# Kernel optimization log

Hardware: AMD Instinct MI355X
Metric: run time of the kernel (lower is better)

The kernel has to match this reference:

```python
import jax, jax.numpy as jnp
import numpy as np

B, N, E = 2, 16384, 262144          # batch, nodes, directed edges (avg deg 16)
K, D, Wm = 256, 3, 1                # nmodes, ndims, nmeasures
C, L, FC = 128, 4, 128              # channels, Fourier layers, fc hidden
IN_DIM, OUT_DIM = 3, 1


def setup_inputs() -> dict:
    key = jax.random.key(0)
    ks = jax.random.split(key, 20)
    s = 1.0 / (C * C)
    inp = {
        "x": jax.random.normal(ks[0], (B, N, IN_DIM), jnp.float32),
        "nodes": jax.random.uniform(ks[1], (B, N, D), jnp.float32),
        "node_mask": jnp.ones((B, N, 1), jnp.float32),
        "node_weights": jax.random.uniform(ks[2], (B, N, Wm), jnp.float32) / N,
        "directed_edges": jax.random.randint(ks[3], (B, E, 2), 0, N),
        "edge_gradient_weights": jax.random.normal(ks[4], (B, E, D), jnp.float32),
        "modes": jax.random.normal(ks[5], (K, D, Wm), jnp.float32),
        "sp_L": jnp.ones((D, Wm), jnp.float32),
        "weights_c": s * jax.random.uniform(ks[6], (L, C, C, K, Wm), jnp.float32),
        "weights_s": s * jax.random.uniform(ks[7], (L, C, C, K, Wm), jnp.float32),
        "weights_0": s * jax.random.uniform(ks[8], (L, C, C, 1, Wm), jnp.float32),
        "fc0_w": jax.random.normal(ks[9], (C, IN_DIM), jnp.float32) * 0.1,
        "fc0_b": jnp.zeros((C,), jnp.float32),
        "ws_w": jax.random.normal(ks[10], (L, C, C), jnp.float32) * 0.05,
        "ws_b": jnp.zeros((L, C), jnp.float32),
        "gws_w": jax.random.normal(ks[11], (L, C, D * C), jnp.float32) * 0.05,
        "gws_b": jnp.zeros((L, C), jnp.float32),
        "fc1_w": jax.random.normal(ks[12], (FC, C), jnp.float32) * 0.05,
        "fc1_b": jnp.zeros((FC,), jnp.float32),
        "fc2_w": jax.random.normal(ks[13], (OUT_DIM, FC), jnp.float32) * 0.05,
        "fc2_b": jnp.zeros((OUT_DIM,), jnp.float32),
    }
    return inp


def _gelu(x):
    return jax.nn.gelu(x, approximate=False)  # torch F.gelu default = exact erf


def _compute_gradient(f, directed_edges, edge_gradient_weights):
    # f: [B, C, N] -> gradients [B, C*D, N] via directed-edge scatter-add
    fT = jnp.transpose(f, (0, 2, 1))                       # [B, N, C]
    tgt, src = directed_edges[..., 0], directed_edges[..., 1]
    f_src = jnp.take_along_axis(fT, src[..., None], axis=1)  # [B, E, C]
    f_tgt = jnp.take_along_axis(fT, tgt[..., None], axis=1)
    msg = jnp.einsum('bed,bec->becd', edge_gradient_weights, f_src - f_tgt)
    msg = msg.reshape(msg.shape[0], msg.shape[1], -1)        # [B, E, C*D]

    def scat(m, t):
        return jnp.zeros((fT.shape[1], m.shape[-1]), m.dtype).at[t].add(m)

    g = jax.vmap(scat)(msg, tgt)                             # [B, N, C*D]
    return jnp.transpose(g, (0, 2, 1))


def _spectral_conv(x, wc, wsn, w0, bc, bs, b0, wbc, wbs, wb0):
    # x: [B, C_in, N]
    xc = jnp.einsum('bix,bxkw->bikw', x, wbc)
    xs = -jnp.einsum('bix,bxkw->bikw', x, wbs)
    x0 = jnp.einsum('bix,bxkw->bikw', x, wb0)
    fc = jnp.einsum('bikw,iokw->bokw', xc, wc) - jnp.einsum('bikw,iokw->bokw', xs, wsn)
    fs = jnp.einsum('bikw,iokw->bokw', xs, wc) + jnp.einsum('bikw,iokw->bokw', xc, wsn)
    f0 = jnp.einsum('bikw,iokw->bokw', x0, w0)
    return (jnp.einsum('bokw,bxkw->box', f0, b0)
            + 2.0 * jnp.einsum('bokw,bxkw->box', fc, bc)
            - 2.0 * jnp.einsum('bokw,bxkw->box', fs, bs))


def reference(x, nodes, node_mask, node_weights, directed_edges, edge_gradient_weights,
              modes, sp_L, weights_c, weights_s, weights_0,
              fc0_w, fc0_b, ws_w, ws_b, gws_w, gws_b, fc1_w, fc1_b, fc2_w, fc2_b):
    # Fourier bases with learnable length-scale sp_L: [K,D,Wm]*[D,Wm]
    temp = jnp.einsum('bxd,kdw->bxkw', nodes, modes * sp_L)   # [B,N,K,Wm]
    bc, bs = jnp.cos(temp), jnp.sin(temp)
    b0 = jnp.zeros((temp.shape[0], temp.shape[1], 1, temp.shape[3]), temp.dtype)
    nw = (node_weights * node_mask)[:, :, None, :]            # [B,N,1,Wm]
    wbc, wbs, wb0 = bc * nw, bs * nw, b0 * nw

    h = jnp.einsum('bxi,ci->bxc', x, fc0_w) + fc0_b           # lift [B,N,C]
    h = jnp.transpose(h, (0, 2, 1))                           # [B,C,N]

    for i in range(L):
        x1 = _spectral_conv(h, weights_c[i], weights_s[i], weights_0[i],
                            bc, bs, b0, wbc, wbs, wb0)
        x2 = jnp.einsum('oc,bcn->bon', ws_w[i], h) + ws_b[i][None, :, None]
        grad = _compute_gradient(h, directed_edges, edge_gradient_weights)
        x3 = jnp.einsum('og,bgn->bon', gws_w[i], grad) + gws_b[i][None, :, None]
        h = x1 + x2 + x3
        if i != L - 1:
            h = _gelu(h)

    h = jnp.transpose(h, (0, 2, 1))                           # [B,N,C]
    h = _gelu(jnp.einsum('bnc,fc->bnf', h, fc1_w) + fc1_b)
    out = jnp.einsum('bnf,of->bno', h, fc2_w) + fc2_b         # [B,N,out_dim]
    return out
```

## Files before the change

kernel.cpp:

```cpp
#include <hip/hip_runtime.h>
#include <math.h>

#define Bn 2
#define Nn 16384
#define En 262144
#define Kn 256
#define Cn 128
#define Rn 512
#define Ln 4
#define LDP 72
#define NSPLIT 32

typedef float f32x4 __attribute__((ext_vector_type(4)));
typedef short s16x8 __attribute__((ext_vector_type(8)));

__device__ __forceinline__ float gelu_f(float x){
  return 0.5f*x*(1.0f + erff(x*0.70710678118654752440f));
}
__device__ __forceinline__ unsigned short f2b(float x){
  unsigned int u = __float_as_uint(x);
  unsigned int r = (u + 0x7FFFu + ((u>>16)&1u)) >> 16;
  return (unsigned short)r;
}
__device__ __forceinline__ float b2f(unsigned short h){
  return __uint_as_float(((unsigned int)h)<<16);
}
__device__ __forceinline__ unsigned int pack2(float lo, float hi){
  return (unsigned int)f2b(lo) | ((unsigned int)f2b(hi) << 16);
}


__global__ __launch_bounds__(256) void k_nw(const float* __restrict__ nwt,
                                            const float* __restrict__ msk,
                                            float* __restrict__ nw){
  int i = blockIdx.x*256 + threadIdx.x;
  nw[i] = nwt[i]*msk[i];
}

__global__ __launch_bounds__(256) void k_basis(const float* __restrict__ nodes,
                                               const float* __restrict__ modes,
                                               const float* __restrict__ spl,
                                               unsigned short* __restrict__ basis,
                                               unsigned short* __restrict__ basisT){
  __shared__ unsigned short tile[32*520];
  int gn0 = blockIdx.x*32;
  int tid = threadIdx.x;
  float m0 = modes[tid*3+0]*spl[0];
  float m1 = modes[tid*3+1]*spl[1];
  float m2 = modes[tid*3+2]*spl[2];
  for (int j=0;j<32;j++){
    const float* nd = nodes + (size_t)(gn0+j)*3;
    float t = nd[0]*m0 + nd[1]*m1 + nd[2]*m2;
    float s,c;
    sincosf(t,&s,&c);
    tile[j*520 + tid]       = f2b(c);
    tile[j*520 + 256 + tid] = f2b(s);
  }
  __syncthreads();
  int row = tid>>3, col0 = (tid&7)*64;
  #pragma unroll
  for (int q=0;q<8;q++){
    s16x8 v = *(const s16x8*)&tile[row*520 + col0 + q*8];
    *(s16x8*)(basis + (size_t)(gn0+row)*Rn + col0 + q*8) = v;
  }
  int b = gn0 >> 14;
  int nl = gn0 & (Nn-1);
  #pragma unroll
  for (int h=0; h<2; h++){
    int r = h*256 + tid;
    unsigned short* dst = basisT + ((size_t)(b*Rn + r))*Nn + nl;
    #pragma unroll
    for (int q=0;q<4;q++){
      unsigned short tmp[8];
      #pragma unroll
      for (int e=0;e<8;e++) tmp[e] = tile[(q*8+e)*520 + r];
      *(s16x8*)(dst + q*8) = *(const s16x8*)tmp;
    }
  }
}

__global__ __launch_bounds__(256) void k_lift(const float* __restrict__ x,
                                              const float* __restrict__ w,
                                              const float* __restrict__ bias,
                                              const float* __restrict__ nw,
                                              unsigned short* __restrict__ hg,
                                              unsigned short* __restrict__ hpack,
                                              unsigned short* __restrict__ hwT){
  __shared__ float ht[64*132];
  int gn0 = blockIdx.x*64;
  int tid = threadIdx.x;
  int c = tid & 127, rh = tid >> 7;
  float w0 = w[c*3], w1 = w[c*3+1], w2 = w[c*3+2], bb = bias[c];
  for (int j=0;j<32;j++){
    int n = rh*32 + j;
    const float* xp = x + (size_t)(gn0+n)*3;
    float v = bb + xp[0]*w0 + xp[1]*w1 + xp[2]*w2;
    ht[n*132 + c] = v;
    unsigned short hv = f2b(v);
    hg[(size_t)(gn0+n)*Rn + c] = hv;
    hpack[(size_t)(gn0+n)*Cn + c] = hv;
  }
  __syncthreads();
  int b = gn0 >> 14, nl = gn0 & (Nn-1);
  int cc = tid>>1, hf = tid&1;
  unsigned short* dst = hwT + ((size_t)(b*Cn + cc))*Nn + nl + hf*32;
  #pragma unroll
  for (int q=0;q<8;q++){
    int n = hf*32 + q*4;
    float4 nv = *(const float4*)&nw[(size_t)b*Nn + nl + n];
    ushort4 pk;
    pk.x = f2b(ht[(n+0)*132+cc]*nv.x);
    pk.y = f2b(ht[(n+1)*132+cc]*nv.y);
    pk.z = f2b(ht[(n+2)*132+cc]*nv.z);
    pk.w = f2b(ht[(n+3)*132+cc]*nv.w);
    *(ushort4*)(dst + q*4) = pk;
  }
}

__global__ __launch_bounds__(128) void k_w2c(const float* __restrict__ ws_w,
                                             const float* __restrict__ ws_b,
                                             const float* __restrict__ gws_w,
                                             const float* __restrict__ gws_b,
                                             unsigned short* __restrict__ W2,
                                             float* __restrict__ bias2){
  int bid = blockIdx.x;
  int tid = threadIdx.x;
  unsigned short* wrow = W2 + (size_t)bid*Rn;
  wrow[tid] = f2b(ws_w[(size_t)bid*Cn + tid]);
  const float* g = gws_w + (size_t)bid*384;
  wrow[128+tid] = f2b(g[tid*3+0]);
  wrow[256+tid] = f2b(g[tid*3+1]);
  wrow[384+tid] = f2b(g[tid*3+2]);
  if (tid==0) bias2[bid] = ws_b[bid] + gws_b[bid];
}

__global__ __launch_bounds__(256) void k_cvt(const float* __restrict__ in,
                                             unsigned short* __restrict__ out, int n){
  int i = blockIdx.x*256 + threadIdx.x;
  if (i < n) out[i] = f2b(in[i]);
}


__global__ __launch_bounds__(256) void k_count(const int* __restrict__ de,
                                               int* __restrict__ cnt){
  int i = blockIdx.x*256 + threadIdx.x;
  int b = i >> 18;
  int tgt = de[(size_t)i*2];
  atomicAdd(&cnt[b*Nn + tgt], 1);
}

__global__ __launch_bounds__(1024) void k_scan(const int* __restrict__ cnt,
                                               int* __restrict__ rowptr,
                                               int* __restrict__ cursor){
  __shared__ int part[1024];
  int t = threadIdx.x;
  int b = t >> 9;
  int li = t & 511;
  int loc[32];
  int s = 0;
  int base = b*Nn + li*32;
  #pragma unroll
  for (int j=0;j<32;j++){ loc[j] = s; s += cnt[base+j]; }
  part[t] = s;
  __syncthreads();
  int run = s;
  for (int off=1; off<512; off<<=1){
    int v = (li >= off) ? part[t-off] : 0;
    __syncthreads();
    part[t] += v;
    __syncthreads();
  }
  int incl = part[t];
  int excl = incl - run;
  int rbase = b*(Nn+1) + li*32;
  #pragma unroll
  for (int j=0;j<32;j++){
    int val = excl + loc[j];
    rowptr[rbase+j] = val;
    cursor[base+j]  = val;
  }
  if (li == 511) rowptr[b*(Nn+1) + Nn] = incl;
}

__global__ __launch_bounds__(256) void k_fill(const int* __restrict__ de,
                                              const float* __restrict__ egw,
                                              int* __restrict__ cursor,
                                              float4* __restrict__ epack){
  int i = blockIdx.x*256 + threadIdx.x;
  int b = i >> 18;
  int tgt = de[(size_t)i*2];
  int src = de[(size_t)i*2+1];
  int pos = atomicAdd(&cursor[b*Nn + tgt], 1);
  const float* g = egw + (size_t)i*3;
  float4 pk;
  pk.x = __int_as_float(src);
  pk.y = g[0]; pk.z = g[1]; pk.w = g[2];
  epack[(size_t)b*En + pos] = pk;
}

__global__ __launch_bounds__(128) void k_grad(const unsigned short* __restrict__ hpack,
                                              const float4* __restrict__ epack,
                                              const int* __restrict__ rowptr,
                                              unsigned short* __restrict__ hg_w){
  int bid = blockIdx.x;
  int b = bid >> 14, n = bid & (Nn-1);
  int tid = threadIdx.x;
  int wv = tid >> 6;
  int l  = tid & 63;
  const unsigned short* hb = hpack + (size_t)b*Nn*Cn;
  unsigned int ft2 = *(const unsigned int*)(hb + (size_t)n*Cn + 2*l);
  float ftlo = b2f((unsigned short)(ft2 & 0xffffu));
  float fthi = b2f((unsigned short)(ft2 >> 16));
  int beg = rowptr[b*(Nn+1) + n];
  int end = rowptr[b*(Nn+1) + n + 1];
  const float4* ep = epack + (size_t)b*En;
  float a0lo=0.f,a0hi=0.f,a1lo=0.f,a1hi=0.f,a2lo=0.f,a2hi=0.f;
  int j = beg + wv;
  for (; j + 2 < end; j += 4){
    float4 pk0 = ep[j];
    float4 pk1 = ep[j+2];
    int s0 = __float_as_int(pk0.x);
    int s1 = __float_as_int(pk1.x);
    unsigned int h0 = *(const unsigned int*)(hb + (size_t)s0*Cn + 2*l);
    unsigned int h1 = *(const unsigned int*)(hb + (size_t)s1*Cn + 2*l);
    float d0lo = b2f((unsigned short)(h0 & 0xffffu)) - ftlo;
    float d0hi = b2f((unsigned short)(h0 >> 16))     - fthi;
    float d1lo = b2f((unsigned short)(h1 & 0xffffu)) - ftlo;
    float d1hi = b2f((unsigned short)(h1 >> 16))     - fthi;
    a0lo += pk0.y*d0lo + pk1.y*d1lo;  a0hi += pk0.y*d0hi + pk1.y*d1hi;
    a1lo += pk0.z*d0lo + pk1.z*d1lo;  a1hi += pk0.z*d0hi + pk1.z*d1hi;
    a2lo += pk0.w*d0lo + pk1.w*d1lo;  a2hi += pk0.w*d0hi + pk1.w*d1hi;
  }
  if (j < end){
    float4 pk = ep[j];
    int src = __float_as_int(pk.x);
    unsigned int hv = *(const unsigned int*)(hb + (size_t)src*Cn + 2*l);
    float dlo = b2f((unsigned short)(hv & 0xffffu)) - ftlo;
    float dhi = b2f((unsigned short)(hv >> 16))     - fthi;
    a0lo += pk.y*dlo; a0hi += pk.y*dhi;
    a1lo += pk.z*dlo; a1hi += pk.z*dhi;
    a2lo += pk.w*dlo; a2hi += pk.w*dhi;
  }
  __shared__ float red[64*7];
  if (wv == 1){
    float* r = &red[l*7];
    r[0]=a0lo; r[1]=a0hi; r[2]=a1lo; r[3]=a1hi; r[4]=a2lo; r[5]=a2hi;
  }
  __syncthreads();
  if (wv == 0){
    const float* r = &red[l*7];
    a0lo+=r[0]; a0hi+=r[1]; a1lo+=r[2]; a1hi+=r[3]; a2lo+=r[4]; a2hi+=r[5];
    unsigned short* o = hg_w + (size_t)bid*Rn + Cn;
    *(unsigned int*)(o + 2*l)       = pack2(a0lo, a0hi);
    *(unsigned int*)(o + 128 + 2*l) = pack2(a1lo, a1hi);
    *(unsigned int*)(o + 256 + 2*l) = pack2(a2lo, a2hi);
  }
}

__device__ __forceinline__ void stage_tile(const unsigned short* __restrict__ g, size_t ldg,
                                           unsigned short* __restrict__ lds, int tid){
  int row = tid >> 3;
  int seg = (tid & 7) * 8;
  #pragma unroll
  for (int rb=0; rb<4; rb++){
    s16x8 v = *(const s16x8*)(g + (size_t)(row + rb*32)*ldg + seg);
    *(s16x8*)(lds + (size_t)(row + rb*32)*LDP + seg) = v;
  }
}

__device__ __forceinline__ void mfma_chunk(const unsigned short* __restrict__ As,
                                           const unsigned short* __restrict__ Bs,
                                           f32x4 acc[4][4], int wm, int wn, int lr, int lg){
  #pragma unroll
  for (int kk=0; kk<2; kk++){
    s16x8 a[4], b[4];
    #pragma unroll
    for (int i=0;i<4;i++)
      a[i] = *(const s16x8*)(As + (size_t)(wm*64 + i*16 + lr)*LDP + kk*32 + lg*8);
    #pragma unroll
    for (int i=0;i<4;i++)
      b[i] = *(const s16x8*)(Bs + (size_t)(wn*64 + i*16 + lr)*LDP + kk*32 + lg*8);
    #pragma unroll
    for (int i=0;i<4;i++)
      #pragma unroll
      for (int j=0;j<4;j++)
        acc[i][j] = __builtin_amdgcn_mfma_f32_16x16x32_bf16(a[i], b[j], acc[i][j], 0, 0, 0);
  }
}

__global__ __launch_bounds__(256) void k_fwd_mfma(const unsigned short* __restrict__ basisT,
                                                  const unsigned short* __restrict__ hwT,
                                                  float* __restrict__ part){
  __shared__ unsigned short As[128*LDP];
  __shared__ unsigned short Bs[128*LDP];
  int tid = threadIdx.x;
  int mt = blockIdx.x;
  int ks = blockIdx.y;
  int b  = blockIdx.z;
  const int KSP = Nn/NSPLIT;
  const unsigned short* A  = basisT + ((size_t)(b*Rn + mt*128))*Nn + (size_t)ks*KSP;
  const unsigned short* Bp = hwT   + ((size_t)(b*Cn))*Nn + (size_t)ks*KSP;
  f32x4 acc[4][4] = {};
  int l = tid & 63, w = tid >> 6, wm = w >> 1, wn = w & 1, lr = l & 15, lg = l >> 4;
  for (int k0 = 0; k0 < KSP; k0 += 64){
    stage_tile(A + k0, Nn, As, tid);
    stage_tile(Bp + k0, Nn, Bs, tid);
    __syncthreads();
    mfma_chunk(As, Bs, acc, wm, wn, lr, lg);
    __syncthreads();
  }
  float* pb = part + ((size_t)ks*Bn + b)*(Cn*Rn);
  int r0 = mt*128 + wm*64;
  int c0 = wn*64;
  #pragma unroll
  for (int i=0;i<4;i++)
    #pragma unroll
    for (int j=0;j<4;j++){
      int r = r0 + i*16 + lg*4;
      int c = c0 + j*16 + lr;
      *(f32x4*)&pb[(size_t)c*Rn + r] = acc[i][j];
    }
}

__global__ __launch_bounds__(256) void k_reduce(const float* __restrict__ part,
                                                float* __restrict__ xf){
  int idx = blockIdx.x*256 + threadIdx.x;
  float s = 0.f;
  #pragma unroll 8
  for (int ks=0; ks<NSPLIT; ks++)
    s += part[(size_t)ks*(Bn*Cn*Rn) + idx];
  xf[idx] = s;
}

__global__ __launch_bounds__(512) void k_mm(const float* __restrict__ xf,
                                            const float* __restrict__ wc,
                                            const float* __restrict__ ws,
                                            float* __restrict__ Fpart){
  int o  = blockIdx.x;
  int is = blockIdx.y;
  int tid = threadIdx.x;
  int half = tid >> 8, t = tid & 255;
  int ibase = is*64 + half*32;
  float fc0=0.f, fs0=0.f, fc1=0.f, fs1=0.f;
  for (int ii=0; ii<32; ii++){
    int i = ibase + ii;
    float wcv = wc[((size_t)i*Cn + o)*Kn + t];
    float wsv = ws[((size_t)i*Cn + o)*Kn + t];
    float x0c = xf[(size_t)i*Rn + t];
    float x0s = xf[(size_t)i*Rn + 256 + t];
    float x1c = xf[(size_t)Cn*Rn + (size_t)i*Rn + t];
    float x1s = xf[(size_t)Cn*Rn + (size_t)i*Rn + 256 + t];
    fc0 += x0c*wcv + x0s*wsv;  fs0 += x0c*wsv - x0s*wcv;
    fc1 += x1c*wcv + x1s*wsv;  fs1 += x1c*wsv - x1s*wcv;
  }
  __shared__ float red[4][256];
  if (half){ red[0][t]=fc0; red[1][t]=fs0; red[2][t]=fc1; red[3][t]=fs1; }
  __syncthreads();
  if (!half){
    fc0 += red[0][t]; fs0 += red[1][t];
    fc1 += red[2][t]; fs1 += red[3][t];
    float* f0 = Fpart + ((size_t)(is*Bn + 0)*Cn + o)*Rn;
    float* f1 = Fpart + ((size_t)(is*Bn + 1)*Cn + o)*Rn;
    f0[t]     = fc0;  f0[256+t] = fs0;
    f1[t]     = fc1;  f1[256+t] = fs1;
  }
}

__global__ __launch_bounds__(256) void k_fcvt(const float* __restrict__ Fpart,
                                              unsigned short* __restrict__ Fbf){
  int idx = blockIdx.x*256 + threadIdx.x;
  float s = Fpart[idx] + Fpart[idx + Bn*Cn*Rn];
  float sc = ((idx & 511) < 256) ? 2.f : -2.f;
  Fbf[idx] = f2b(sc*s);
}

template<int GELU, int WRITE_AUX>
__global__ __launch_bounds__(256) void k_invcomb(const unsigned short* __restrict__ basis,
                                                 const unsigned short* __restrict__ Fbf,
                                                 unsigned short* __restrict__ hg,
                                                 const unsigned short* __restrict__ W2l,
                                                 const float* __restrict__ bias2l,
                                                 const float* __restrict__ nw,
                                                 unsigned short* __restrict__ hpack,
                                                 unsigned short* __restrict__ hwT){
  __shared__ unsigned short As[128*LDP];
  __shared__ unsigned short Bs[128*LDP];
  int tid = threadIdx.x;
  int nt = blockIdx.x;
  int b  = blockIdx.y;
  size_t nbase = (size_t)b*Nn + (size_t)nt*128;
  f32x4 acc[4][4] = {};
  int l = tid & 63, w = tid >> 6, wm = w >> 1, wn = w & 1, lr = l & 15, lg = l >> 4;
  const unsigned short* A1 = basis + nbase*Rn;
  const unsigned short* B1 = Fbf + (size_t)b*Cn*Rn;
  for (int k0=0;k0<512;k0+=64){
    stage_tile(A1+k0, Rn, As, tid);
    stage_tile(B1+k0, Rn, Bs, tid);
    __syncthreads();
    mfma_chunk(As,Bs,acc,wm,wn,lr,lg);
    __syncthreads();
  }
  const unsigned short* A2 = hg + nbase*Rn;
  for (int k0=0;k0<512;k0+=64){
    stage_tile(A2+k0, Rn, As, tid);
    stage_tile(W2l+k0, Rn, Bs, tid);
    __syncthreads();
    mfma_chunk(As,Bs,acc,wm,wn,lr,lg);
    __syncthreads();
  }
  int n0 = wm*64, c0 = wn*64;
  #pragma unroll
  for (int i=0;i<4;i++){
    int nloc = n0 + i*16 + lg*4;
    #pragma unroll
    for (int j=0;j<4;j++){
      int c = c0 + j*16 + lr;
      float bsv = bias2l[c];
      float v[4];
      #pragma unroll
      for (int e=0;e<4;e++){
        v[e] = acc[i][j][e] + bsv;
        if (GELU) v[e] = gelu_f(v[e]);
        unsigned short hv = f2b(v[e]);
        hpack[(nbase + nloc + e)*Cn + c] = hv;
        if (WRITE_AUX) hg[(nbase + nloc + e)*Rn + c] = hv;
      }
      if (WRITE_AUX){
        float4 w4 = *(const float4*)&nw[(size_t)b*Nn + nt*128 + nloc];
        ushort4 pk;
        pk.x = f2b(v[0]*w4.x); pk.y = f2b(v[1]*w4.y);
        pk.z = f2b(v[2]*w4.z); pk.w = f2b(v[3]*w4.w);
        *(ushort4*)&hwT[((size_t)(b*Cn + c))*Nn + nt*128 + nloc] = pk;
      }
    }
  }
}

__global__ __launch_bounds__(256) void k_fc1(const unsigned short* __restrict__ hpack,
                                             const unsigned short* __restrict__ fw,
                                             const float* __restrict__ fb,
                                             unsigned short* __restrict__ h2){
  __shared__ unsigned short As[128*LDP];
  __shared__ unsigned short Bs[128*LDP];
  int tid = threadIdx.x;
  int nt = blockIdx.x;
  int b  = blockIdx.y;
  size_t nbase = (size_t)b*Nn + (size_t)nt*128;
  f32x4 acc[4][4] = {};
  int l = tid & 63, w = tid >> 6, wm = w >> 1, wn = w & 1, lr = l & 15, lg = l >> 4;
  const unsigned short* A = hpack + nbase*Cn;
  for (int k0=0;k0<128;k0+=64){
    stage_tile(A+k0, Cn, As, tid);
    stage_tile(fw+k0, Cn, Bs, tid);
    __syncthreads();
    mfma_chunk(As,Bs,acc,wm,wn,lr,lg);
    __syncthreads();
  }
  int n0 = wm*64, c0 = wn*64;
  #pragma unroll
  for (int i=0;i<4;i++){
    int nloc = n0 + i*16 + lg*4;
    #pragma unroll
    for (int j=0;j<4;j++){
      int c = c0 + j*16 + lr;
      float bsv = fb[c];
      #pragma unroll
      for (int e=0;e<4;e++){
        float v = gelu_f(acc[i][j][e] + bsv);
        h2[(nbase + nloc + e)*Cn + c] = f2b(v);
      }
    }
  }
}

__global__ __launch_bounds__(256) void k_out(const unsigned short* __restrict__ h2,
                                             const float* __restrict__ w,
                                             const float* __restrict__ bptr,
                                             float* __restrict__ outp){
  int tid = threadIdx.x;
  int node = blockIdx.x*4 + (tid>>6);
  int f = tid & 63;
  const unsigned short* hp = h2 + (size_t)node*Cn;
  float s = b2f(hp[f])*w[f] + b2f(hp[f+64])*w[f+64];
  #pragma unroll
  for (int off=32; off>0; off>>=1) s += __shfl_down(s, off);
  if (f==0) outp[node] = s + bptr[0];
}

static constexpr size_t OB_BASIS  = 0;
static constexpr size_t OB_BASIST = OB_BASIS  + 33554432;
static constexpr size_t OB_HG     = OB_BASIST + 33554432;
static constexpr size_t OB_HWT    = OB_HG     + 33554432;
static constexpr size_t OB_H2     = OB_HWT    + 8388608;
static constexpr size_t OB_HP     = OB_H2     + 8388608;
static constexpr size_t OB_NW     = OB_HP     + 8388608;
static constexpr size_t OB_XF     = OB_NW     + 131072;
static constexpr size_t OB_FBF    = OB_XF     + 524288;
static constexpr size_t OB_FPART  = OB_FBF    + 262144;
static constexpr size_t OB_W2     = OB_FPART  + 1048576;
static constexpr size_t OB_B2     = OB_W2     + 524288;
static constexpr size_t OB_FC1W   = OB_B2     + 2048;
static constexpr size_t OB_EPACK  = OB_FC1W   + 32768;
static constexpr size_t OB_INT    = OB_EPACK  + 8388608;
static constexpr size_t OB_PART   = OB_INT    + 524288;

extern "C" void kernel_launch(void* const* d_in, const int* in_sizes, int n_in,
                              void* d_out, int out_size, void* d_ws, size_t ws_size,
                              hipStream_t stream) {
  const float* x            = (const float*)d_in[0];
  const float* nodes        = (const float*)d_in[1];
  const float* node_mask    = (const float*)d_in[2];
  const float* node_weights = (const float*)d_in[3];
  const int*   de           = (const int*)  d_in[4];
  const float* egw          = (const float*)d_in[5];
  const float* modes        = (const float*)d_in[6];
  const float* spl          = (const float*)d_in[7];
  const float* wc           = (const float*)d_in[8];
  const float* wsp          = (const float*)d_in[9];
  const float* fc0_w        = (const float*)d_in[11];
  const float* fc0_b        = (const float*)d_in[12];
  const float* ws_w         = (const float*)d_in[13];
  const float* ws_b         = (const float*)d_in[14];
  const float* gws_w        = (const float*)d_in[15];
  const float* gws_b        = (const float*)d_in[16];
  const float* fc1_w        = (const float*)d_in[17];
  const float* fc1_b        = (const float*)d_in[18];
  const float* fc2_w        = (const float*)d_in[19];
  const float* fc2_b        = (const float*)d_in[20];
  float* outp = (float*)d_out;

  char* wsb = (char*)d_ws;
  unsigned short* basis  = (unsigned short*)(wsb + OB_BASIS);
  unsigned short* basisT = (unsigned short*)(wsb + OB_BASIST);
  unsigned short* hg     = (unsigned short*)(wsb + OB_HG);
  unsigned short* hwT    = (unsigned short*)(wsb + OB_HWT);
  unsigned short* h2     = (unsigned short*)(wsb + OB_H2);
  unsigned short* hpack  = (unsigned short*)(wsb + OB_HP);
  float* nw              = (float*)(wsb + OB_NW);
  float* xf              = (float*)(wsb + OB_XF);
  unsigned short* Fbf    = (unsigned short*)(wsb + OB_FBF);
  float* Fpart           = (float*)(wsb + OB_FPART);
  unsigned short* W2     = (unsigned short*)(wsb + OB_W2);
  float* bias2           = (float*)(wsb + OB_B2);
  unsigned short* fc1wb  = (unsigned short*)(wsb + OB_FC1W);
  float4* epack          = (float4*)(wsb + OB_EPACK);
  int* count  = (int*)(wsb + OB_INT);
  int* rowptr = count + Bn*Nn;
  int* cursor = rowptr + Bn*(Nn+1);
  float* part = (float*)(wsb + OB_PART);

  k_nw<<<(Bn*Nn)/256, 256, 0, stream>>>(node_weights, node_mask, nw);
  k_basis<<<(Bn*Nn)/32, 256, 0, stream>>>(nodes, modes, spl, basis, basisT);
  k_lift<<<(Bn*Nn)/64, 256, 0, stream>>>(x, fc0_w, fc0_b, nw, hg, hpack, hwT);

  (void)hipMemsetAsync(count, 0, (size_t)Bn*Nn*sizeof(int), stream);
  k_count<<<(Bn*En)/256, 256, 0, stream>>>(de, count);
  k_scan<<<1, 1024, 0, stream>>>(count, rowptr, cursor);
  k_fill<<<(Bn*En)/256, 256, 0, stream>>>(de, egw, cursor, epack);

  k_w2c<<<Ln*Cn, 128, 0, stream>>>(ws_w, ws_b, gws_w, gws_b, W2, bias2);
  k_cvt<<<64, 256, 0, stream>>>(fc1_w, fc1wb, Cn*Cn);

  for (int l=0; l<Ln; l++){
    k_fwd_mfma<<<dim3(4,NSPLIT,2), 256, 0, stream>>>(basisT, hwT, part);
    k_reduce<<<(Bn*Cn*Rn)/256, 256, 0, stream>>>(part, xf);
    k_mm<<<dim3(Cn,2), 512, 0, stream>>>(xf, wc + (size_t)l*Cn*Cn*Kn,
                                         wsp + (size_t)l*Cn*Cn*Kn, Fpart);
    k_fcvt<<<(Bn*Cn*Rn)/256, 256, 0, stream>>>(Fpart, Fbf);
    k_grad<<<Bn*Nn, 128, 0, stream>>>(hpack, epack, rowptr, hg);
    if (l < Ln-1){
      k_invcomb<1,1><<<dim3(Nn/128,2), 256, 0, stream>>>(
          basis, Fbf, hg, W2 + (size_t)l*Cn*Rn, bias2 + l*Cn, nw, hpack, hwT);
    } else {
      k_invcomb<0,0><<<dim3(Nn/128,2), 256, 0, stream>>>(
          basis, Fbf, hg, W2 + (size_t)l*Cn*Rn, bias2 + l*Cn, nw, hpack, hwT);
    }
  }

  k_fc1<<<dim3(Nn/128,2), 256, 0, stream>>>(hpack, fc1wb, fc1_b, h2);
  k_out<<<(Bn*Nn)/4, 256, 0, stream>>>(h2, fc2_w, fc2_b, outp);
}
```

Baseline: 545.1 us.

## Use eight-wave blocks for inverse/combine and fc1 GEMMs, double forward split-K

The inverse-transform/combine and fc1 GEMM kernels now launch 512 threads in eight waves, each wave owning a 64x32 output tile instead of 64x64. This halves per-wave accumulators and doubles the waves per block, since only 256 blocks cover the device. The two K-loops of the combine kernel are merged into one loop that stages both operand pairs into separate shared buffers, so there are half as many barriers at the cost of twice the shared memory. The forward GEMM split-K count is doubled to put more blocks in flight, which adds partial-sum traffic for the reduction.

```diff
diff --git a/kernel.cpp b/kernel.cpp
--- a/kernel.cpp
+++ b/kernel.cpp
@@ -9,7 +9,7 @@
 #define Rn 512
 #define Ln 4
 #define LDP 72
-#define NSPLIT 32
+#define NSPLIT 64
 
 typedef float f32x4 __attribute__((ext_vector_type(4)));
 typedef short s16x8 __attribute__((ext_vector_type(8)));
@@ -267,6 +267,16 @@
     *(s16x8*)(lds + (size_t)(row + rb*32)*LDP + seg) = v;
   }
 }
+__device__ __forceinline__ void stage_tile512(const unsigned short* __restrict__ g, size_t ldg,
+                                              unsigned short* __restrict__ lds, int tid){
+  int row = tid >> 3;
+  int seg = (tid & 7) * 8;
+  #pragma unroll
+  for (int rb=0; rb<2; rb++){
+    s16x8 v = *(const s16x8*)(g + (size_t)(row + rb*64)*ldg + seg);
+    *(s16x8*)(lds + (size_t)(row + rb*64)*LDP + seg) = v;
+  }
+}
 
 __device__ __forceinline__ void mfma_chunk(const unsigned short* __restrict__ As,
                                            const unsigned short* __restrict__ Bs,
@@ -284,6 +294,26 @@
     for (int i=0;i<4;i++)
       #pragma unroll
       for (int j=0;j<4;j++)
+        acc[i][j] = __builtin_amdgcn_mfma_f32_16x16x32_bf16(a[i], b[j], acc[i][j], 0, 0, 0);
+  }
+}
+
+__device__ __forceinline__ void mfma_chunk8(const unsigned short* __restrict__ As,
+                                            const unsigned short* __restrict__ Bs,
+                                            f32x4 acc[4][2], int wm, int wn, int lr, int lg){
+  #pragma unroll
+  for (int kk=0; kk<2; kk++){
+    s16x8 a[4], b[2];
+    #pragma unroll
+    for (int i=0;i<4;i++)
+      a[i] = *(const s16x8*)(As + (size_t)(wm*64 + i*16 + lr)*LDP + kk*32 + lg*8);
+    #pragma unroll
+    for (int j=0;j<2;j++)
+      b[j] = *(const s16x8*)(Bs + (size_t)(wn*32 + j*16 + lr)*LDP + kk*32 + lg*8);
+    #pragma unroll
+    for (int i=0;i<4;i++)
+      #pragma unroll
+      for (int j=0;j<2;j++)
         acc[i][j] = __builtin_amdgcn_mfma_f32_16x16x32_bf16(a[i], b[j], acc[i][j], 0, 0, 0);
   }
 }
@@ -375,7 +405,7 @@
 }
 
 template<int GELU, int WRITE_AUX>
-__global__ __launch_bounds__(256) void k_invcomb(const unsigned short* __restrict__ basis,
+__global__ __launch_bounds__(512) void k_invcomb(const unsigned short* __restrict__ basis,
                                                  const unsigned short* __restrict__ Fbf,
                                                  unsigned short* __restrict__ hg,
                                                  const unsigned short* __restrict__ W2l,
@@ -383,38 +413,37 @@
                                                  const float* __restrict__ nw,
                                                  unsigned short* __restrict__ hpack,
                                                  unsigned short* __restrict__ hwT){
-  __shared__ unsigned short As[128*LDP];
-  __shared__ unsigned short Bs[128*LDP];
+  __shared__ unsigned short As1[128*LDP];
+  __shared__ unsigned short Bs1[128*LDP];
+  __shared__ unsigned short As2[128*LDP];
+  __shared__ unsigned short Bs2[128*LDP];
   int tid = threadIdx.x;
   int nt = blockIdx.x;
   int b  = blockIdx.y;
   size_t nbase = (size_t)b*Nn + (size_t)nt*128;
-  f32x4 acc[4][4] = {};
-  int l = tid & 63, w = tid >> 6, wm = w >> 1, wn = w & 1, lr = l & 15, lg = l >> 4;
+  f32x4 acc[4][2] = {};
+  int l = tid & 63, w = tid >> 6, wm = w >> 2, wn = w & 3, lr = l & 15, lg = l >> 4;
   const unsigned short* A1 = basis + nbase*Rn;
   const unsigned short* B1 = Fbf + (size_t)b*Cn*Rn;
-  for (int k0=0;k0<512;k0+=64){
-    stage_tile(A1+k0, Rn, As, tid);
-    stage_tile(B1+k0, Rn, Bs, tid);
-    __syncthreads();
-    mfma_chunk(As,Bs,acc,wm,wn,lr,lg);
-    __syncthreads();
-  }
   const unsigned short* A2 = hg + nbase*Rn;
   for (int k0=0;k0<512;k0+=64){
-    stage_tile(A2+k0, Rn, As, tid);
-    stage_tile(W2l+k0, Rn, Bs, tid);
-    __syncthreads();
-    mfma_chunk(As,Bs,acc,wm,wn,lr,lg);
-    __syncthreads();
-  }
-  int n0 = wm*64, c0 = wn*64;
+    stage_tile512(A1+k0, Rn, As1, tid);
+    stage_tile512(B1+k0, Rn, Bs1, tid);
+    stage_tile512(A2+k0, Rn, As2, tid);
+    stage_tile512(W2l+k0, Rn, Bs2, tid);
+    __syncthreads();
+    mfma_chunk8(As1,Bs1,acc,wm,wn,lr,lg);
+    mfma_chunk8(As2,Bs2,acc,wm,wn,lr,lg);
+    __syncthreads();
+  }
   #pragma unroll
   for (int i=0;i<4;i++){
-    int nloc = n0 + i*16 + lg*4;
-    #pragma unroll
-    for (int j=0;j<4;j++){
-      int c = c0 + j*16 + lr;
+    int nloc = wm*64 + i*16 + lg*4;
+    float4 w4;
+    if (WRITE_AUX) w4 = *(const float4*)&nw[(size_t)b*Nn + nt*128 + nloc];
+    #pragma unroll
+    for (int j=0;j<2;j++){
+      int c = wn*32 + j*16 + lr;
       float bsv = bias2l[c];
       float v[4];
       #pragma unroll
@@ -426,7 +455,6 @@
         if (WRITE_AUX) hg[(nbase + nloc + e)*Rn + c] = hv;
       }
       if (WRITE_AUX){
-        float4 w4 = *(const float4*)&nw[(size_t)b*Nn + nt*128 + nloc];
         ushort4 pk;
         pk.x = f2b(v[0]*w4.x); pk.y = f2b(v[1]*w4.y);
         pk.z = f2b(v[2]*w4.z); pk.w = f2b(v[3]*w4.w);
@@ -436,7 +464,7 @@
   }
 }
 
-__global__ __launch_bounds__(256) void k_fc1(const unsigned short* __restrict__ hpack,
+__global__ __launch_bounds__(512) void k_fc1(const unsigned short* __restrict__ hpack,
                                              const unsigned short* __restrict__ fw,
                                              const float* __restrict__ fb,
                                              unsigned short* __restrict__ h2){
@@ -446,23 +474,22 @@
   int nt = blockIdx.x;
   int b  = blockIdx.y;
   size_t nbase = (size_t)b*Nn + (size_t)nt*128;
-  f32x4 acc[4][4] = {};
-  int l = tid & 63, w = tid >> 6, wm = w >> 1, wn = w & 1, lr = l & 15, lg = l >> 4;
+  f32x4 acc[4][2] = {};
+  int l = tid & 63, w = tid >> 6, wm = w >> 2, wn = w & 3, lr = l & 15, lg = l >> 4;
   const unsigned short* A = hpack + nbase*Cn;
   for (int k0=0;k0<128;k0+=64){
-    stage_tile(A+k0, Cn, As, tid);
-    stage_tile(fw+k0, Cn, Bs, tid);
-    __syncthreads();
-    mfma_chunk(As,Bs,acc,wm,wn,lr,lg);
-    __syncthreads();
-  }
-  int n0 = wm*64, c0 = wn*64;
+    stage_tile512(A+k0, Cn, As, tid);
+    stage_tile512(fw+k0, Cn, Bs, tid);
+    __syncthreads();
+    mfma_chunk8(As,Bs,acc,wm,wn,lr,lg);
+    __syncthreads();
+  }
   #pragma unroll
   for (int i=0;i<4;i++){
-    int nloc = n0 + i*16 + lg*4;
-    #pragma unroll
-    for (int j=0;j<4;j++){
-      int c = c0 + j*16 + lr;
+    int nloc = wm*64 + i*16 + lg*4;
+    #pragma unroll
+    for (int j=0;j<2;j++){
+      int c = wn*32 + j*16 + lr;
       float bsv = fb[c];
       #pragma unroll
       for (int e=0;e<4;e++){
@@ -569,14 +596,14 @@
     k_fcvt<<<(Bn*Cn*Rn)/256, 256, 0, stream>>>(Fpart, Fbf);
     k_grad<<<Bn*Nn, 128, 0, stream>>>(hpack, epack, rowptr, hg);
     if (l < Ln-1){
-      k_invcomb<1,1><<<dim3(Nn/128,2), 256, 0, stream>>>(
+      k_invcomb<1,1><<<dim3(Nn/128,2), 512, 0, stream>>>(
           basis, Fbf, hg, W2 + (size_t)l*Cn*Rn, bias2 + l*Cn, nw, hpack, hwT);
     } else {
-      k_invcomb<0,0><<<dim3(Nn/128,2), 256, 0, stream>>>(
+      k_invcomb<0,0><<<dim3(Nn/128,2), 512, 0, stream>>>(
           basis, Fbf, hg, W2 + (size_t)l*Cn*Rn, bias2 + l*Cn, nw, hpack, hwT);
     }
   }
 
-  k_fc1<<<dim3(Nn/128,2), 256, 0, stream>>>(hpack, fc1wb, fc1_b, h2);
+  k_fc1<<<dim3(Nn/128,2), 512, 0, stream>>>(hpack, fc1wb, fc1_b, h2);
   k_out<<<(Bn*Nn)/4, 256, 0, stream>>>(h2, fc2_w, fc2_b, outp);
 }
```

Result: faster. 534.2 us (-2.0%).
